# Kernel optimization log

Measured on AMD Instinct MI355X. Metric: run time of the kernel, lower is better.

Reference implementation:

```python
import jax, jax.numpy as jnp
import numpy as np

M, N, D, H, E = 100000, 50000, 128, 2, 1000000
NEG_SLOPE = 0.2  # standard GAT LeakyReLU slope


def setup_inputs() -> dict:
    key = jax.random.key(0)
    ks = jax.random.split(key, 14)
    inp = {
        "u_prev": jax.random.normal(ks[0], (M, D), jnp.float32),
        "i_prev": jax.random.normal(ks[1], (N, D), jnp.float32),
        "w_user": jax.random.normal(ks[2], (D, D), jnp.float32) * 0.05,
        "b_user": jax.random.normal(ks[3], (D,), jnp.float32) * 0.05,
        "w_item": jax.random.normal(ks[4], (D, D), jnp.float32) * 0.05,
        "b_item": jax.random.normal(ks[5], (D,), jnp.float32) * 0.05,
        "a_u_src": jax.random.normal(ks[6], (H, D), jnp.float32) * 0.1,
        "a_u_dst": jax.random.normal(ks[7], (H, D), jnp.float32) * 0.1,
        "a_i_src": jax.random.normal(ks[8], (H, D), jnp.float32) * 0.1,
        "a_i_dst": jax.random.normal(ks[9], (H, D), jnp.float32) * 0.1,
        "u2i_row": jax.random.randint(ks[10], (E,), 0, M, jnp.int32),
        "u2i_col": jax.random.randint(ks[11], (E,), 0, N, jnp.int32),
        "i2u_row": jax.random.randint(ks[12], (E,), 0, N, jnp.int32),
        "i2u_col": jax.random.randint(ks[13], (E,), 0, M, jnp.int32),
    }
    return inp


def _segment_softmax(logits, seg, num_segments):
    # neighborhood softmax: normalize per adjacency row
    mx = jax.ops.segment_max(logits, seg, num_segments=num_segments)
    e = jnp.exp(logits - mx[seg])
    s = jax.ops.segment_sum(e, seg, num_segments=num_segments)
    return e / s[seg]


def _attend(row, col, h_src, h_dst, a_src, a_dst, num_src):
    hs = h_src[row]  # (E, D) gather of source-node features
    hd = h_dst[col]  # (E, D) gather of dest-node features
    head_outs = []
    for h in range(a_src.shape[0]):  # small fixed head count
        logits = jax.nn.leaky_relu(hs @ a_src[h] + hd @ a_dst[h], NEG_SLOPE)  # (E,)
        att = _segment_softmax(logits, row, num_src)                         # (E,)
        # sparse att @ h_dst == row-segment sum of att-weighted neighbor features
        head_outs.append(jax.ops.segment_sum(att[:, None] * hd, row, num_segments=num_src))
    out = sum(head_outs) / len(head_outs)  # reduce_att = mean over heads
    return jax.nn.elu(out)                  # self.nonlinear


def reference(u_prev, i_prev, w_user, b_user, w_item, b_item,
              a_u_src, a_u_dst, a_i_src, a_i_dst,
              u2i_row, u2i_col, i2u_row, i2u_col):
    u = u_prev @ w_user + b_user  # (M, D)
    i = i_prev @ w_item + b_item  # (N, D)
    u_next = _attend(u2i_row, u2i_col, u, i, a_u_src, a_u_dst, M)
    i_next = _attend(i2u_row, i2u_col, i, u, a_i_src, a_i_dst, N)
    return (u_next, i_next)
```

## Files before the change

kernel.cpp:

```cpp
#include <hip/hip_runtime.h>
#include <cstdint>
#include <cstddef>

#define D 128
#define NEG_SLOPE 0.2f
#define CAP 64

__device__ __forceinline__ float lrelu(float x) { return x > 0.0f ? x : NEG_SLOPE * x; }
__device__ __forceinline__ float elu_f(float x) { return x > 0.0f ? x : expm1f(x); }
__device__ __forceinline__ unsigned short f2bf(float f) {
    unsigned u = __float_as_uint(f);
    return (unsigned short)((u + 0x7fffu + ((u >> 16) & 1u)) >> 16);
}

typedef __attribute__((ext_vector_type(8))) short bf16x8;
typedef __attribute__((ext_vector_type(4))) float f32x4;

__global__ __launch_bounds__(256) void prep_w(const float* __restrict__ Wu,
                                              const float* __restrict__ Wi,
                                              unsigned short* __restrict__ WswU,
                                              unsigned short* __restrict__ WswI)
{
    bool di = (int)blockIdx.x >= 8;
    const float* W = di ? Wi : Wu;
    unsigned short* Wsw = di ? WswI : WswU;
    int c = ((int)blockIdx.x & 7) * 256 + (int)threadIdx.x;
    int n = c >> 4, s = c & 15;
    const float* src = W + (size_t)(s * 8) * D + n;
    unsigned t0 = ((unsigned)f2bf(src[0 * D])) | ((unsigned)f2bf(src[1 * D]) << 16);
    unsigned t1 = ((unsigned)f2bf(src[2 * D])) | ((unsigned)f2bf(src[3 * D]) << 16);
    unsigned t2 = ((unsigned)f2bf(src[4 * D])) | ((unsigned)f2bf(src[5 * D]) << 16);
    unsigned t3 = ((unsigned)f2bf(src[6 * D])) | ((unsigned)f2bf(src[7 * D]) << 16);
    *(uint4*)((char*)Wsw + n * 256 + ((s * 16) ^ ((n & 7) << 4))) = make_uint4(t0, t1, t2, t3);
}

struct GemmDir {
    const float* A; const unsigned short* Wsw; const float* bias;
    const float* v0; const float* v1; const float* v2; const float* v3;
    unsigned short* Cb;
    float4* att; int R;
};

__global__ __launch_bounds__(256) void gemm_att(GemmDir g0, int nb0, GemmDir g1)
{
    int gb = blockIdx.x;
    const bool second = gb >= nb0;
    GemmDir g = second ? g1 : g0;
    const int bid = second ? (gb - nb0) : gb;

    __shared__ unsigned short Wl[128 * 128];

    const int tid = threadIdx.x;
    const int row0 = bid * 64;
    const int wave = tid >> 6;
    const int lane = tid & 63;
    const int lm = lane & 15;
    const int lg = lane >> 4;

    {
        const uint4* wsrc = (const uint4*)g.Wsw;
#pragma unroll
        for (int q = 0; q < 8; ++q) {
            int c = tid + q * 256;
            *(uint4*)((char*)Wl + (size_t)c * 16) = wsrc[c];
        }
    }
    __syncthreads();

    int ar = row0 + (wave << 4) + lm;
    if (ar > g.R - 1) ar = g.R - 1;
    const float* Arow = g.A + (size_t)ar * D;

    f32x4 acc[8];
#pragma unroll
    for (int nt = 0; nt < 8; ++nt) { acc[nt][0] = 0.f; acc[nt][1] = 0.f; acc[nt][2] = 0.f; acc[nt][3] = 0.f; }

    const int xr = (lm & 7) << 4;
#pragma unroll
    for (int ks = 0; ks < 4; ++ks) {
        const float4 a0 = *(const float4*)(Arow + ks * 32 + lg * 8);
        const float4 a1 = *(const float4*)(Arow + ks * 32 + lg * 8 + 4);
        bf16x8 af;
        af[0] = (short)f2bf(a0.x); af[1] = (short)f2bf(a0.y);
        af[2] = (short)f2bf(a0.z); af[3] = (short)f2bf(a0.w);
        af[4] = (short)f2bf(a1.x); af[5] = (short)f2bf(a1.y);
        af[6] = (short)f2bf(a1.z); af[7] = (short)f2bf(a1.w);
        const int slot = ks * 4 + lg;
        const char* bbase = (const char*)Wl + lm * 256 + ((slot * 16) ^ xr);
#pragma unroll
        for (int nt = 0; nt < 8; ++nt) {
            bf16x8 wf = *(const bf16x8*)(bbase + nt * 4096);
            acc[nt] = __builtin_amdgcn_mfma_f32_16x16x32_bf16(wf, af, acc[nt], 0, 0, 0);
        }
    }

    const int colb = lg << 2;
    const int row = row0 + (wave << 4) + lm;
    const bool valid = row < g.R;

#pragma unroll
    for (int nt = 0; nt < 8; ++nt) {
        float4 bv = *(const float4*)(g.bias + nt * 16 + colb);
        acc[nt][0] += bv.x; acc[nt][1] += bv.y; acc[nt][2] += bv.z; acc[nt][3] += bv.w;
    }
    if (valid) {
#pragma unroll
        for (int nt = 0; nt < 8; ++nt) {
            ushort4 s = { f2bf(acc[nt][0]), f2bf(acc[nt][1]), f2bf(acc[nt][2]), f2bf(acc[nt][3]) };
            *(ushort4*)(g.Cb + (size_t)row * D + nt * 16 + colb) = s;
        }
    }

    const float* vs[4] = { g.v0, g.v1, g.v2, g.v3 };
    float p[4];
#pragma unroll
    for (int h = 0; h < 4; ++h) {
        float s = 0.f;
#pragma unroll
        for (int nt = 0; nt < 8; ++nt) {
            float4 vh = *(const float4*)(vs[h] + nt * 16 + colb);
            s += acc[nt][0] * vh.x + acc[nt][1] * vh.y + acc[nt][2] * vh.z + acc[nt][3] * vh.w;
        }
        p[h] = s;
    }
#pragma unroll
    for (int h = 0; h < 4; ++h) {
        p[h] += __shfl_xor(p[h], 16, 64);
        p[h] += __shfl_xor(p[h], 32, 64);
    }
    if (lg == 0 && valid) g.att[row] = make_float4(p[0], p[1], p[2], p[3]);
}

__global__ __launch_bounds__(256) void scatter_fill(
    const int* __restrict__ rowA, const int* __restrict__ colA,
    int* __restrict__ cntA, int* __restrict__ slotA, int EA, int chunkA,
    const int* __restrict__ rowB, const int* __restrict__ colB,
    int* __restrict__ cntB, int* __restrict__ slotB, int EB, int chunkB)
{
    int half = gridDim.x >> 1;
    bool dB = (int)blockIdx.x >= half;
    int b = dB ? (int)blockIdx.x - half : (int)blockIdx.x;
    const int* row = dB ? rowB : rowA;
    const int* col = dB ? colB : colA;
    int* cnt  = dB ? cntB : cntA;
    int* slot = dB ? slotB : slotA;
    int E = dB ? EB : EA;
    int chunk = dB ? chunkB : chunkA;

    int part = b & 7;
    int idx  = b >> 3;
    int nper = half >> 3;
    int lo = part * chunk, hi = lo + chunk;

    for (int i = idx * 256 + (int)threadIdx.x; i < E; i += nper * 256) {
        int r = row[i];
        if (r >= lo && r < hi) {
            int pos = atomicAdd(&cnt[r], 1);
            if (pos < CAP) slot[(size_t)r * CAP + pos] = col[i];
        }
    }
}

__device__ __forceinline__ void aggregate_row(
    const int* __restrict__ cnt, const int* __restrict__ slot,
    const char* __restrict__ satt, const char* __restrict__ datt,
    const unsigned short* __restrict__ featb,
    float* __restrict__ out, int seg, int lane)
{
    int deg = cnt[seg];
    deg = deg > CAP ? CAP : deg;
    float2 sa = *(const float2*)(satt + (size_t)seg * 16);
    float accx = 0.0f, accy = 0.0f;
    if (deg > 0) {
        int myc = 0;
        float e0 = 0.0f, e1 = 0.0f;
        if (lane < deg) {
            myc = slot[(size_t)seg * CAP + lane];
            float2 da = *(const float2*)(datt + (size_t)myc * 16);
            e0 = __expf(lrelu(sa.x + da.x));
            e1 = __expf(lrelu(sa.y + da.y));
        }
        float s0 = e0, s1 = e1;
#pragma unroll
        for (int o = 32; o > 0; o >>= 1) {
            s0 += __shfl_xor(s0, o, 64);
            s1 += __shfl_xor(s1, o, 64);
        }
        float myw = e0 * (0.5f / s0) + e1 * (0.5f / s1);
        float a0x = 0.f, a0y = 0.f, a1x = 0.f, a1y = 0.f,
              a2x = 0.f, a2y = 0.f, a3x = 0.f, a3y = 0.f;
        int j = 0;
        for (; j + 4 <= deg; j += 4) {
            int c0 = __shfl(myc, j, 64), c1 = __shfl(myc, j + 1, 64);
            int c2 = __shfl(myc, j + 2, 64), c3 = __shfl(myc, j + 3, 64);
            float w0 = __shfl(myw, j, 64), w1 = __shfl(myw, j + 1, 64);
            float w2 = __shfl(myw, j + 2, 64), w3 = __shfl(myw, j + 3, 64);
            unsigned f0 = *(const unsigned*)(featb + (size_t)c0 * D + 2 * lane);
            unsigned f1 = *(const unsigned*)(featb + (size_t)c1 * D + 2 * lane);
            unsigned f2 = *(const unsigned*)(featb + (size_t)c2 * D + 2 * lane);
            unsigned f3 = *(const unsigned*)(featb + (size_t)c3 * D + 2 * lane);
            a0x += w0 * __uint_as_float(f0 << 16); a0y += w0 * __uint_as_float(f0 & 0xffff0000u);
            a1x += w1 * __uint_as_float(f1 << 16); a1y += w1 * __uint_as_float(f1 & 0xffff0000u);
            a2x += w2 * __uint_as_float(f2 << 16); a2y += w2 * __uint_as_float(f2 & 0xffff0000u);
            a3x += w3 * __uint_as_float(f3 << 16); a3y += w3 * __uint_as_float(f3 & 0xffff0000u);
        }
        for (; j < deg; ++j) {
            int c0 = __shfl(myc, j, 64);
            float w0 = __shfl(myw, j, 64);
            unsigned f0 = *(const unsigned*)(featb + (size_t)c0 * D + 2 * lane);
            a0x += w0 * __uint_as_float(f0 << 16); a0y += w0 * __uint_as_float(f0 & 0xffff0000u);
        }
        accx = (a0x + a1x) + (a2x + a3x);
        accy = (a0y + a1y) + (a2y + a3y);
    }
    *(float2*)(out + (size_t)seg * D + 2 * lane) = make_float2(elu_f(accx), elu_f(accy));
}

__global__ __launch_bounds__(256) void aggregate_both(
    const int* cntA, const int* slotA, const char* sattA, const char* dattA,
    const unsigned short* featA, float* outA, int SA, int nbA,
    const int* cntB, const int* slotB, const char* sattB, const char* dattB,
    const unsigned short* featB, float* outB, int SB)
{
    int lane = threadIdx.x & 63;
    if (blockIdx.x < (unsigned)nbA) {
        int seg = blockIdx.x * 4 + (threadIdx.x >> 6);
        if (seg < SA) aggregate_row(cntA, slotA, sattA, dattA, featA, outA, seg, lane);
    } else {
        int seg = (blockIdx.x - nbA) * 4 + (threadIdx.x >> 6);
        if (seg < SB) aggregate_row(cntB, slotB, sattB, dattB, featB, outB, seg, lane);
    }
}

extern "C" void kernel_launch(void* const* d_in, const int* in_sizes, int n_in,
                              void* d_out, int out_size, void* d_ws, size_t ws_size,
                              hipStream_t stream)
{
    const float* u_prev  = (const float*)d_in[0];
    const float* i_prev  = (const float*)d_in[1];
    const float* w_user  = (const float*)d_in[2];
    const float* b_user  = (const float*)d_in[3];
    const float* w_item  = (const float*)d_in[4];
    const float* b_item  = (const float*)d_in[5];
    const float* a_u_src = (const float*)d_in[6];
    const float* a_u_dst = (const float*)d_in[7];
    const float* a_i_src = (const float*)d_in[8];
    const float* a_i_dst = (const float*)d_in[9];
    const int* u2i_row = (const int*)d_in[10];
    const int* u2i_col = (const int*)d_in[11];
    const int* i2u_row = (const int*)d_in[12];
    const int* i2u_col = (const int*)d_in[13];

    const int M = in_sizes[0] / D;
    const int N = in_sizes[1] / D;
    const int EA = in_sizes[10];
    const int EB = in_sizes[12];

    char* ws = (char*)d_ws;
    size_t off = 0;
    auto carve = [&](size_t bytes) -> char* {
        char* p = ws + off;
        off += (bytes + 255) & ~(size_t)255;
        return p;
    };
    unsigned short* u_featb = (unsigned short*)carve((size_t)M * D * 2);
    unsigned short* i_featb = (unsigned short*)carve((size_t)N * D * 2);
    float4* u_att   = (float4*)carve((size_t)M * 16);
    float4* i_att   = (float4*)carve((size_t)N * 16);
    int*    cntA    = (int*)carve((size_t)M * 4);
    int*    cntB    = (int*)carve((size_t)N * 4);
    int*    slotA   = (int*)carve((size_t)M * CAP * 4);
    int*    slotB   = (int*)carve((size_t)N * CAP * 4);
    unsigned short* wswU = (unsigned short*)carve((size_t)D * D * 2);
    unsigned short* wswI = (unsigned short*)carve((size_t)D * D * 2);
    (void)ws_size; (void)n_in; (void)out_size;

    hipMemsetAsync(cntA, 0, (size_t)M * 4, stream);
    hipMemsetAsync(cntB, 0, (size_t)N * 4, stream);

    prep_w<<<16, 256, 0, stream>>>(w_user, w_item, wswU, wswI);

    GemmDir gu = { u_prev, wswU, b_user, a_u_src, a_u_src + D, a_i_dst, a_i_dst + D, u_featb, u_att, M };
    GemmDir gi = { i_prev, wswI, b_item, a_u_dst, a_u_dst + D, a_i_src, a_i_src + D, i_featb, i_att, N };
    int nbGu = (M + 63) / 64, nbGi = (N + 63) / 64;
    gemm_att<<<nbGu + nbGi, 256, 0, stream>>>(gu, nbGu, gi);

    int chunkA = (M + 7) / 8, chunkB = (N + 7) / 8;
    scatter_fill<<<2048, 256, 0, stream>>>(u2i_row, u2i_col, cntA, slotA, EA, chunkA,
                                           i2u_row, i2u_col, cntB, slotB, EB, chunkB);

    float* out_u = (float*)d_out;
    float* out_i = out_u + (size_t)M * D;
    int nbAggA = (M + 3) / 4, nbAggB = (N + 3) / 4;
    aggregate_both<<<nbAggA + nbAggB, 256, 0, stream>>>(
        cntA, slotA, (const char*)u_att, (const char*)i_att, i_featb, out_u, M, nbAggA,
        cntB, slotB, (const char*)i_att + 8, (const char*)u_att + 8, u_featb, out_i, N);
}
```

Baseline: 395.5 us.

## Co-schedule edge scatter with GEMM blocks and use 16-byte gathers in aggregation

The separate scatter_fill launch is folded into the GEMM kernel as extra leading blocks (512 scatter blocks instead of 2048), so slot filling and the projection GEMM can run concurrently and one launch is saved. The aggregation now has each 16-lane group process a different neighbour using 16-byte bf16 loads, then reduces across the four groups with shuffles. This is meant to issue fewer, wider gather loads and to overlap the atomic-bound scatter with the compute-bound GEMM. The cost is fewer scatter blocks doing more iterations each, plus padded tail iterations and a cross-group shuffle reduction in aggregation.

```diff
diff --git a/kernel.cpp b/kernel.cpp
--- a/kernel.cpp
+++ b/kernel.cpp
@@ -41,9 +41,39 @@
     float4* att; int R;
 };
 
-__global__ __launch_bounds__(256) void gemm_att(GemmDir g0, int nb0, GemmDir g1)
-{
-    int gb = blockIdx.x;
+__global__ __launch_bounds__(256) void gemm_att_scatter(
+    GemmDir g0, int nb0, GemmDir g1,
+    const int* __restrict__ rowA, const int* __restrict__ colA,
+    int* __restrict__ cntA, int* __restrict__ slotA, int EA, int chunkA,
+    const int* __restrict__ rowB, const int* __restrict__ colB,
+    int* __restrict__ cntB, int* __restrict__ slotB, int EB, int chunkB,
+    int scatHalf)
+{
+    int nbScat = 2 * scatHalf;
+    if ((int)blockIdx.x < nbScat) {
+        bool dB = (int)blockIdx.x >= scatHalf;
+        int b = dB ? (int)blockIdx.x - scatHalf : (int)blockIdx.x;
+        const int* row = dB ? rowB : rowA;
+        const int* col = dB ? colB : colA;
+        int* cnt  = dB ? cntB : cntA;
+        int* slot = dB ? slotB : slotA;
+        int E = dB ? EB : EA;
+        int chunk = dB ? chunkB : chunkA;
+        int part = b & 7;
+        int idx  = b >> 3;
+        int nper = scatHalf >> 3;
+        int lo = part * chunk, hi = lo + chunk;
+        for (int i = idx * 256 + (int)threadIdx.x; i < E; i += nper * 256) {
+            int r = row[i];
+            if (r >= lo && r < hi) {
+                int pos = atomicAdd(&cnt[r], 1);
+                if (pos < CAP) slot[(size_t)r * CAP + pos] = col[i];
+            }
+        }
+        return;
+    }
+
+    int gb = blockIdx.x - nbScat;
     const bool second = gb >= nb0;
     GemmDir g = second ? g1 : g0;
     const int bid = second ? (gb - nb0) : gb;
@@ -131,36 +161,6 @@
     if (lg == 0 && valid) g.att[row] = make_float4(p[0], p[1], p[2], p[3]);
 }
 
-__global__ __launch_bounds__(256) void scatter_fill(
-    const int* __restrict__ rowA, const int* __restrict__ colA,
-    int* __restrict__ cntA, int* __restrict__ slotA, int EA, int chunkA,
-    const int* __restrict__ rowB, const int* __restrict__ colB,
-    int* __restrict__ cntB, int* __restrict__ slotB, int EB, int chunkB)
-{
-    int half = gridDim.x >> 1;
-    bool dB = (int)blockIdx.x >= half;
-    int b = dB ? (int)blockIdx.x - half : (int)blockIdx.x;
-    const int* row = dB ? rowB : rowA;
-    const int* col = dB ? colB : colA;
-    int* cnt  = dB ? cntB : cntA;
-    int* slot = dB ? slotB : slotA;
-    int E = dB ? EB : EA;
-    int chunk = dB ? chunkB : chunkA;
-
-    int part = b & 7;
-    int idx  = b >> 3;
-    int nper = half >> 3;
-    int lo = part * chunk, hi = lo + chunk;
-
-    for (int i = idx * 256 + (int)threadIdx.x; i < E; i += nper * 256) {
-        int r = row[i];
-        if (r >= lo && r < hi) {
-            int pos = atomicAdd(&cnt[r], 1);
-            if (pos < CAP) slot[(size_t)r * CAP + pos] = col[i];
-        }
-    }
-}
-
 __device__ __forceinline__ void aggregate_row(
     const int* __restrict__ cnt, const int* __restrict__ slot,
     const char* __restrict__ satt, const char* __restrict__ datt,
@@ -170,7 +170,12 @@
     int deg = cnt[seg];
     deg = deg > CAP ? CAP : deg;
     float2 sa = *(const float2*)(satt + (size_t)seg * 16);
-    float accx = 0.0f, accy = 0.0f;
+    const int grp = lane >> 4;
+    const int lm = lane & 15;
+    float acc[8];
+#pragma unroll
+    for (int k = 0; k < 8; ++k) acc[k] = 0.0f;
+
     if (deg > 0) {
         int myc = 0;
         float e0 = 0.0f, e1 = 0.0f;
@@ -187,33 +192,35 @@
             s1 += __shfl_xor(s1, o, 64);
         }
         float myw = e0 * (0.5f / s0) + e1 * (0.5f / s1);
-        float a0x = 0.f, a0y = 0.f, a1x = 0.f, a1y = 0.f,
-              a2x = 0.f, a2y = 0.f, a3x = 0.f, a3y = 0.f;
-        int j = 0;
-        for (; j + 4 <= deg; j += 4) {
-            int c0 = __shfl(myc, j, 64), c1 = __shfl(myc, j + 1, 64);
-            int c2 = __shfl(myc, j + 2, 64), c3 = __shfl(myc, j + 3, 64);
-            float w0 = __shfl(myw, j, 64), w1 = __shfl(myw, j + 1, 64);
-            float w2 = __shfl(myw, j + 2, 64), w3 = __shfl(myw, j + 3, 64);
-            unsigned f0 = *(const unsigned*)(featb + (size_t)c0 * D + 2 * lane);
-            unsigned f1 = *(const unsigned*)(featb + (size_t)c1 * D + 2 * lane);
-            unsigned f2 = *(const unsigned*)(featb + (size_t)c2 * D + 2 * lane);
-            unsigned f3 = *(const unsigned*)(featb + (size_t)c3 * D + 2 * lane);
-            a0x += w0 * __uint_as_float(f0 << 16); a0y += w0 * __uint_as_float(f0 & 0xffff0000u);
-            a1x += w1 * __uint_as_float(f1 << 16); a1y += w1 * __uint_as_float(f1 & 0xffff0000u);
-            a2x += w2 * __uint_as_float(f2 << 16); a2y += w2 * __uint_as_float(f2 & 0xffff0000u);
-            a3x += w3 * __uint_as_float(f3 << 16); a3y += w3 * __uint_as_float(f3 & 0xffff0000u);
-        }
-        for (; j < deg; ++j) {
-            int c0 = __shfl(myc, j, 64);
-            float w0 = __shfl(myw, j, 64);
-            unsigned f0 = *(const unsigned*)(featb + (size_t)c0 * D + 2 * lane);
-            a0x += w0 * __uint_as_float(f0 << 16); a0y += w0 * __uint_as_float(f0 & 0xffff0000u);
-        }
-        accx = (a0x + a1x) + (a2x + a3x);
-        accy = (a0y + a1y) + (a2y + a3y);
-    }
-    *(float2*)(out + (size_t)seg * D + 2 * lane) = make_float2(elu_f(accx), elu_f(accy));
+
+        for (int j = 0; j < deg; j += 4) {
+            int idx = j + grp;
+            int sidx = idx < deg ? idx : (deg - 1);
+            int cc = __shfl(myc, sidx, 64);
+            float ww = __shfl(myw, sidx, 64);
+            if (idx >= deg) ww = 0.0f;
+            uint4 f = *(const uint4*)(featb + (size_t)cc * D + lm * 8);
+            acc[0] += ww * __uint_as_float(f.x << 16);
+            acc[1] += ww * __uint_as_float(f.x & 0xffff0000u);
+            acc[2] += ww * __uint_as_float(f.y << 16);
+            acc[3] += ww * __uint_as_float(f.y & 0xffff0000u);
+            acc[4] += ww * __uint_as_float(f.z << 16);
+            acc[5] += ww * __uint_as_float(f.z & 0xffff0000u);
+            acc[6] += ww * __uint_as_float(f.w << 16);
+            acc[7] += ww * __uint_as_float(f.w & 0xffff0000u);
+        }
+#pragma unroll
+        for (int k = 0; k < 8; ++k) {
+            acc[k] += __shfl_xor(acc[k], 16, 64);
+            acc[k] += __shfl_xor(acc[k], 32, 64);
+        }
+    }
+    if (grp == 0) {
+        float4 o0 = make_float4(elu_f(acc[0]), elu_f(acc[1]), elu_f(acc[2]), elu_f(acc[3]));
+        float4 o1 = make_float4(elu_f(acc[4]), elu_f(acc[5]), elu_f(acc[6]), elu_f(acc[7]));
+        *(float4*)(out + (size_t)seg * D + lm * 8) = o0;
+        *(float4*)(out + (size_t)seg * D + lm * 8 + 4) = o1;
+    }
 }
 
 __global__ __launch_bounds__(256) void aggregate_both(
@@ -283,11 +290,12 @@
     GemmDir gu = { u_prev, wswU, b_user, a_u_src, a_u_src + D, a_i_dst, a_i_dst + D, u_featb, u_att, M };
     GemmDir gi = { i_prev, wswI, b_item, a_u_dst, a_u_dst + D, a_i_src, a_i_src + D, i_featb, i_att, N };
     int nbGu = (M + 63) / 64, nbGi = (N + 63) / 64;
-    gemm_att<<<nbGu + nbGi, 256, 0, stream>>>(gu, nbGu, gi);
-
     int chunkA = (M + 7) / 8, chunkB = (N + 7) / 8;
-    scatter_fill<<<2048, 256, 0, stream>>>(u2i_row, u2i_col, cntA, slotA, EA, chunkA,
-                                           i2u_row, i2u_col, cntB, slotB, EB, chunkB);
+    int scatHalf = 256;
+    gemm_att_scatter<<<2 * scatHalf + nbGu + nbGi, 256, 0, stream>>>(
+        gu, nbGu, gi,
+        u2i_row, u2i_col, cntA, slotA, EA, chunkA,
+        i2u_row, i2u_col, cntB, slotB, EB, chunkB, scatHalf);
 
     float* out_u = (float*)d_out;
     float* out_i = out_u + (size_t)M * D;
```

After: 465.4 us. +17.7%, slower.
